# Performance work log

Hardware: AMD Instinct MI355X
Metric: run time of the kernel (lower is better)

## Reference

```python
import jax, jax.numpy as jnp
import numpy as np

N = 50000
E = 800000
D_IN = 128
D_H = 128
N_CLASSES = 40
N_HIDDEN = 2


def _gcn_norm(edge_index, num_nodes):
    # Add self loops, compute symmetric normalization D^-1/2 (A+I) D^-1/2
    loops = jnp.arange(num_nodes, dtype=edge_index.dtype)
    src = jnp.concatenate([edge_index[0], loops])
    dst = jnp.concatenate([edge_index[1], loops])
    deg = jax.ops.segment_sum(jnp.ones_like(src, dtype=jnp.float32), dst,
                              num_segments=num_nodes)
    dinv = jnp.where(deg > 0, jax.lax.rsqrt(jnp.maximum(deg, 1.0)), 0.0)
    norm = dinv[src] * dinv[dst]  # [E+N]
    return src, dst, norm


def _gcn_conv(x, src, dst, norm, W, b):
    h = x @ W                          # [N, d_out] transform first (PyG order)
    msg = h[src] * norm[:, None]       # gather + scale, [E+N, d_out]
    out = jax.ops.segment_sum(msg, dst, num_segments=x.shape[0])
    return out + b


def setup_inputs() -> dict:
    key = jax.random.key(0)
    ks = jax.random.split(key, 8)
    x = jax.random.normal(ks[0], (N, D_IN), dtype=jnp.float32)
    edge_index = jax.random.randint(ks[1], (2, E), 0, N, dtype=jnp.int64)
    s = 1.0 / np.sqrt(D_IN)
    W1 = jax.random.uniform(ks[2], (D_IN, D_H), minval=-s, maxval=s, dtype=jnp.float32)
    b1 = jnp.zeros((D_H,), dtype=jnp.float32)
    sh = 1.0 / np.sqrt(D_H)
    Wh = jax.random.uniform(ks[3], (N_HIDDEN, D_H, D_H), minval=-sh, maxval=sh, dtype=jnp.float32)
    bh = jnp.zeros((N_HIDDEN, D_H), dtype=jnp.float32)
    Wf = jax.random.uniform(ks[4], (D_H, N_CLASSES), minval=-sh, maxval=sh, dtype=jnp.float32)
    bf = jnp.zeros((N_CLASSES,), dtype=jnp.float32)
    return {"x": x, "edge_index": edge_index, "W1": W1, "b1": b1,
            "Wh": Wh, "bh": bh, "Wf": Wf, "bf": bf}


def reference(x, edge_index, W1, b1, Wh, bh, Wf, bf):
    src, dst, norm = _gcn_norm(edge_index, x.shape[0])
    h = jax.nn.relu(_gcn_conv(x, src, dst, norm, W1, b1))
    for i in range(Wh.shape[0]):  # small fixed layer count
        h = jax.nn.relu(_gcn_conv(h, src, dst, norm, Wh[i], bh[i]))
    # extra relu in original forward is a no-op after relu above
    return h @ Wf + bf
```

## Files before the change

### kernel.cpp

```cpp
#include <hip/hip_runtime.h>

#define D 128
#define NC 40

typedef __attribute__((ext_vector_type(8))) short short8v;
typedef __attribute__((ext_vector_type(4))) float f32x4;

__device__ __forceinline__ unsigned short f2bf(float f) {
    unsigned u = __float_as_uint(f);
    u += 0x7fff + ((u >> 16) & 1);
    return (unsigned short)(u >> 16);
}
__device__ __forceinline__ float bf2f(unsigned short h) {
    return __uint_as_float(((unsigned)h) << 16);
}

__device__ __forceinline__ int load_idx(const int* ei, long long pos, int is64) {
    return is64 ? ei[pos * 2] : ei[pos];
}

__device__ __forceinline__ int detect64(const int* __restrict__ ei) {
    int lane = threadIdx.x & 63;
    int hi = ei[lane * 2 + 1];
    return __any(hi != 0) ? 0 : 1;
}


__global__ void count_convert_kernel(const int* __restrict__ ei, int* __restrict__ deg,
                                     int E, int EB,
                                     const float* __restrict__ W1, const float* __restrict__ Wh,
                                     const float* __restrict__ Wf,
                                     unsigned short* __restrict__ Wc1, unsigned short* __restrict__ Wch0,
                                     unsigned short* __restrict__ Wch1, unsigned short* __restrict__ Wcf) {
    if (blockIdx.x < EB) {
        int is64 = detect64(ei);
        int e = blockIdx.x * 256 + threadIdx.x;
        if (e < E) {
            int d = load_idx(ei, (long long)E + e, is64);
            atomicAdd(&deg[d], 1);
        }
    } else {
        int idx = (blockIdx.x - EB) * 256 + threadIdx.x;
        if (idx < 49152) {
            int which = idx >> 14;
            int j = idx & 16383;
            int nn = j >> 7, k = j & 127;
            const float* W = (which == 0) ? W1 : (which == 1) ? Wh : Wh + 16384;
            unsigned short* o = (which == 0) ? Wc1 : (which == 1) ? Wch0 : Wch1;
            float v = W[k * 128 + nn];
            unsigned short h = f2bf(v);
            o[j] = h;
            o[16384 + j] = f2bf(v - bf2f(h));
        } else if (idx < 49152 + 6144) {
            int j = idx - 49152;
            int nn = j >> 7, k = j & 127;
            float v = (nn < NC) ? Wf[k * NC + nn] : 0.f;
            unsigned short h = f2bf(v);
            Wcf[j] = h;
            Wcf[6144 + j] = f2bf(v - bf2f(h));
        }
    }
}

__global__ void scan1_kernel(const int* __restrict__ deg, int* __restrict__ bsum, int m) {
    int i = blockIdx.x * 512 + threadIdx.x;
    int v = (i < m) ? deg[i] : 0;
    #pragma unroll
    for (int off = 32; off; off >>= 1) v += __shfl_down(v, off, 64);
    __shared__ int ws[8];
    if ((threadIdx.x & 63) == 0) ws[threadIdx.x >> 6] = v;
    __syncthreads();
    if (threadIdx.x == 0) {
        int s = 0;
        #pragma unroll
        for (int j = 0; j < 8; ++j) s += ws[j];
        bsum[blockIdx.x] = s;
    }
}

__global__ void scan3_kernel(const int* __restrict__ deg, const int* __restrict__ bsum,
                             int* __restrict__ rowptr, int* __restrict__ fill,
                             float* __restrict__ dinv, int n, int E, int nb) {
    int t = threadIdx.x;
    int lane = t & 63, w = t >> 6;
    int pv = (t < nb && t < (int)blockIdx.x) ? bsum[t] : 0;
    int rs = pv;
    #pragma unroll
    for (int off = 32; off; off >>= 1) rs += __shfl_down(rs, off, 64);
    __shared__ int red[8];
    if (lane == 0) red[w] = rs;
    __syncthreads();
    int base = 0;
    #pragma unroll
    for (int j = 0; j < 8; ++j) base += red[j];
    __syncthreads();

    int i = blockIdx.x * 512 + t;
    int v = (i < n) ? deg[i] : 0;
    int s = v;
    #pragma unroll
    for (int off = 1; off < 64; off <<= 1) {
        int x = __shfl_up(s, off, 64);
        if (lane >= off) s += x;
    }
    __shared__ int wsum[8];
    if (lane == 63) wsum[w] = s;
    __syncthreads();
    int wbase = 0;
    #pragma unroll
    for (int j = 0; j < 8; ++j) if (j < w) wbase += wsum[j];
    int excl = base + wbase + s - v;
    if (i < n) {
        rowptr[i] = excl;
        fill[i]   = excl;
        dinv[i]   = rsqrtf((float)(v + 1));
    }
    if (i == 0) rowptr[n] = E;
}

__global__ void scatter_kernel(const int* __restrict__ ei, int* __restrict__ fill,
                               const float* __restrict__ dinv, int2* __restrict__ col2, int E) {
    int is64 = detect64(ei);
    int e = blockIdx.x * 256 + threadIdx.x;
    if (e >= E) return;
    int s = load_idx(ei, (long long)e, is64);
    int d = load_idx(ei, (long long)E + e, is64);
    int pos = atomicAdd(&fill[d], 1);
    col2[pos] = make_int2(s, __float_as_int(dinv[s]));
}

__launch_bounds__(256)
__global__ void fused_layer_kernel(const float4* __restrict__ h4,
                                   const unsigned short* __restrict__ Wcvt,
                                   const float* __restrict__ bias,
                                   const float* __restrict__ dinv,
                                   const int* __restrict__ rowptr, const int2* __restrict__ col2,
                                   float* __restrict__ out, int n) {
    __shared__ unsigned short Ah[16 * 128];
    __shared__ unsigned short Al[16 * 128];
    int t = threadIdx.x;
    int g = t >> 4, l16 = t & 15;
    int node = blockIdx.x * 16 + g;
    int nd = (node < n) ? node : (n - 1);
    float dn = dinv[nd];
    size_t rowbase = (size_t)nd * 32;

    float4 a0 = h4[rowbase + l16];
    float4 a1 = h4[rowbase + l16 + 16];
    float4 acc0, acc1;
    acc0.x = a0.x * dn; acc0.y = a0.y * dn; acc0.z = a0.z * dn; acc0.w = a0.w * dn;
    acc1.x = a1.x * dn; acc1.y = a1.y * dn; acc1.z = a1.z * dn; acc1.w = a1.w * dn;

    int e = rowptr[nd], e1 = rowptr[nd + 1];
    for (; e + 4 <= e1; e += 4) {
        int2 c[4];
        #pragma unroll
        for (int j = 0; j < 4; ++j) c[j] = col2[e + j];
        float4 v0[4], v1[4];
        #pragma unroll
        for (int j = 0; j < 4; ++j) {
            size_t b = (size_t)c[j].x * 32;
            v0[j] = h4[b + l16];
            v1[j] = h4[b + l16 + 16];
        }
        #pragma unroll
        for (int j = 0; j < 4; ++j) {
            float ds = __int_as_float(c[j].y);
            acc0.x += v0[j].x * ds; acc0.y += v0[j].y * ds;
            acc0.z += v0[j].z * ds; acc0.w += v0[j].w * ds;
            acc1.x += v1[j].x * ds; acc1.y += v1[j].y * ds;
            acc1.z += v1[j].z * ds; acc1.w += v1[j].w * ds;
        }
    }
    for (; e < e1; ++e) {
        int2 c = col2[e];
        float ds = __int_as_float(c.y);
        size_t b = (size_t)c.x * 32;
        float4 v0 = h4[b + l16], v1 = h4[b + l16 + 16];
        acc0.x += v0.x * ds; acc0.y += v0.y * ds; acc0.z += v0.z * ds; acc0.w += v0.w * ds;
        acc1.x += v1.x * ds; acc1.y += v1.y * ds; acc1.z += v1.z * ds; acc1.w += v1.w * ds;
    }
    acc0.x *= dn; acc0.y *= dn; acc0.z *= dn; acc0.w *= dn;
    acc1.x *= dn; acc1.y *= dn; acc1.z *= dn; acc1.w *= dn;

    {
        int kc0 = l16 >> 1, sub = (l16 & 1) * 8;
        int off0 = (g << 8) + (((kc0) << 4) ^ ((g & 7) << 4)) + sub;
        int off1 = (g << 8) + (((kc0 + 8) << 4) ^ ((g & 7) << 4)) + sub;
        ushort4 h0, l0, h1, l1;
        h0.x = f2bf(acc0.x); l0.x = f2bf(acc0.x - bf2f(h0.x));
        h0.y = f2bf(acc0.y); l0.y = f2bf(acc0.y - bf2f(h0.y));
        h0.z = f2bf(acc0.z); l0.z = f2bf(acc0.z - bf2f(h0.z));
        h0.w = f2bf(acc0.w); l0.w = f2bf(acc0.w - bf2f(h0.w));
        h1.x = f2bf(acc1.x); l1.x = f2bf(acc1.x - bf2f(h1.x));
        h1.y = f2bf(acc1.y); l1.y = f2bf(acc1.y - bf2f(h1.y));
        h1.z = f2bf(acc1.z); l1.z = f2bf(acc1.z - bf2f(h1.z));
        h1.w = f2bf(acc1.w); l1.w = f2bf(acc1.w - bf2f(h1.w));
        *(ushort4*)((char*)Ah + off0) = h0;
        *(ushort4*)((char*)Al + off0) = l0;
        *(ushort4*)((char*)Ah + off1) = h1;
        *(ushort4*)((char*)Al + off1) = l1;
    }
    __syncthreads();

    int l = t & 63, wv = t >> 6;
    int lr = l & 15, lh = l >> 4;
    const unsigned short* Whi = Wcvt;
    const unsigned short* Wlo = Wcvt + 128 * 128;
    f32x4 o0 = (f32x4){0.f, 0.f, 0.f, 0.f};
    f32x4 o1 = (f32x4){0.f, 0.f, 0.f, 0.f};
    int n0 = wv * 32;
    #pragma unroll
    for (int ks = 0; ks < 4; ++ks) {
        int aoff = (lr << 8) + (((ks << 6) + (lh << 4)) ^ ((lr & 7) << 4));
        short8v ah = *(short8v*)((char*)Ah + aoff);
        short8v al = *(short8v*)((char*)Al + aoff);
        int c0 = (n0 + lr) * 128 + ks * 32 + lh * 8;
        int c1 = (n0 + 16 + lr) * 128 + ks * 32 + lh * 8;
        short8v bh0 = *(const short8v*)&Whi[c0];
        short8v bl0 = *(const short8v*)&Wlo[c0];
        short8v bh1 = *(const short8v*)&Whi[c1];
        short8v bl1 = *(const short8v*)&Wlo[c1];
        o0 = __builtin_amdgcn_mfma_f32_16x16x32_bf16(ah, bh0, o0, 0, 0, 0);
        o0 = __builtin_amdgcn_mfma_f32_16x16x32_bf16(ah, bl0, o0, 0, 0, 0);
        o0 = __builtin_amdgcn_mfma_f32_16x16x32_bf16(al, bh0, o0, 0, 0, 0);
        o1 = __builtin_amdgcn_mfma_f32_16x16x32_bf16(ah, bh1, o1, 0, 0, 0);
        o1 = __builtin_amdgcn_mfma_f32_16x16x32_bf16(ah, bl1, o1, 0, 0, 0);
        o1 = __builtin_amdgcn_mfma_f32_16x16x32_bf16(al, bh1, o1, 0, 0, 0);
    }
    float b0 = bias[n0 + lr], b1v = bias[n0 + 16 + lr];
    #pragma unroll
    for (int r = 0; r < 4; ++r) {
        int row = blockIdx.x * 16 + lh * 4 + r;
        if (row < n) {
            out[(size_t)row * 128 + n0 + lr]      = fmaxf(o0[r] + b0, 0.f);
            out[(size_t)row * 128 + n0 + 16 + lr] = fmaxf(o1[r] + b1v, 0.f);
        }
    }
}

__launch_bounds__(256)
__global__ void final_mfma_kernel(const float* __restrict__ A, const unsigned short* __restrict__ Wcvt,
                                  const float* __restrict__ bf, float* __restrict__ C, int M) {
    __shared__ unsigned short Ah[64 * 128];
    __shared__ unsigned short Al[64 * 128];
    int t = threadIdx.x;
    int l = t & 63, w = t >> 6;
    int lr = l & 15, lh = l >> 4;

    const unsigned short* Whi = Wcvt;
    const unsigned short* Wlo = Wcvt + 48 * 128;
    short8v bhi[3][4], blo[3][4];
    #pragma unroll
    for (int nt = 0; nt < 3; ++nt) {
        int n = nt * 16 + lr;
        #pragma unroll
        for (int ks = 0; ks < 4; ++ks) {
            bhi[nt][ks] = *(const short8v*)&Whi[n * 128 + ks * 32 + lh * 8];
            blo[nt][ks] = *(const short8v*)&Wlo[n * 128 + ks * 32 + lh * 8];
        }
    }

    int row0 = blockIdx.x * 64;
    #pragma unroll
    for (int c = 0; c < 4; ++c) {
        int chunk = c * 256 + t;
        int r  = chunk >> 4;
        int kc = chunk & 15;
        int gr = row0 + r; if (gr >= M) gr = M - 1;
        float4 a0 = *(const float4*)&A[(size_t)gr * 128 + kc * 8];
        float4 a1 = *(const float4*)&A[(size_t)gr * 128 + kc * 8 + 4];
        float av[8] = {a0.x, a0.y, a0.z, a0.w, a1.x, a1.y, a1.z, a1.w};
        short8v hv, lv;
        #pragma unroll
        for (int j = 0; j < 8; ++j) {
            unsigned short hi = f2bf(av[j]);
            hv[j] = (short)hi;
            lv[j] = (short)f2bf(av[j] - bf2f(hi));
        }
        int off = (r << 8) + ((kc << 4) ^ ((r & 7) << 4));
        *(short8v*)((char*)Ah + off) = hv;
        *(short8v*)((char*)Al + off) = lv;
    }
    __syncthreads();

    f32x4 acc[3];
    #pragma unroll
    for (int nt = 0; nt < 3; ++nt) acc[nt] = (f32x4){0.f, 0.f, 0.f, 0.f};
    int row = w * 16 + lr;
    #pragma unroll
    for (int ks = 0; ks < 4; ++ks) {
        int off = (row << 8) + (((ks << 6) + (lh << 4)) ^ ((row & 7) << 4));
        short8v ah = *(short8v*)((char*)Ah + off);
        short8v al = *(short8v*)((char*)Al + off);
        #pragma unroll
        for (int nt = 0; nt < 3; ++nt) {
            acc[nt] = __builtin_amdgcn_mfma_f32_16x16x32_bf16(ah, bhi[nt][ks], acc[nt], 0, 0, 0);
            acc[nt] = __builtin_amdgcn_mfma_f32_16x16x32_bf16(ah, blo[nt][ks], acc[nt], 0, 0, 0);
            acc[nt] = __builtin_amdgcn_mfma_f32_16x16x32_bf16(al, bhi[nt][ks], acc[nt], 0, 0, 0);
        }
    }
    #pragma unroll
    for (int nt = 0; nt < 3; ++nt) {
        int col = nt * 16 + lr;
        #pragma unroll
        for (int r = 0; r < 4; ++r) {
            int ro = row0 + w * 16 + lh * 4 + r;
            if (col < NC && ro < M) C[(size_t)ro * NC + col] = acc[nt][r] + bf[col];
        }
    }
}

extern "C" void kernel_launch(void* const* d_in, const int* in_sizes, int n_in,
                              void* d_out, int out_size, void* d_ws, size_t ws_size,
                              hipStream_t stream) {
    const float* x  = (const float*)d_in[0];
    const int*   ei = (const int*)d_in[1];
    const float* W1 = (const float*)d_in[2];
    const float* b1 = (const float*)d_in[3];
    const float* Wh = (const float*)d_in[4];
    const float* bh = (const float*)d_in[5];
    const float* Wf = (const float*)d_in[6];
    const float* bf = (const float*)d_in[7];
    float* out = (float*)d_out;

    int n = in_sizes[0] / D;
    int E = in_sizes[1] / 2;

    char* ws = (char*)d_ws;
    size_t off = 0;
    auto alloc = [&](size_t bytes) {
        void* p = ws + off;
        off = (off + bytes + 255) & ~(size_t)255;
        return p;
    };
    float* B0     = (float*)alloc((size_t)n * D * 4);
    float* B1     = (float*)alloc((size_t)n * D * 4);
    int*   deg    = (int*)alloc((size_t)n * 4);
    int*   rowptr = (int*)alloc((size_t)(n + 1) * 4);
    int*   fill   = (int*)alloc((size_t)n * 4);
    int2*  col2   = (int2*)alloc((size_t)E * 8);
    float* dinv   = (float*)alloc((size_t)n * 4);
    int*   bsum   = (int*)alloc(1024 * 4);
    unsigned short* Wc1  = (unsigned short*)alloc(2 * 128 * 128 * 2);
    unsigned short* Wch0 = (unsigned short*)alloc(2 * 128 * 128 * 2);
    unsigned short* Wch1 = (unsigned short*)alloc(2 * 128 * 128 * 2);
    unsigned short* Wcf  = (unsigned short*)alloc(2 * 48 * 128 * 2);

    int EB = (E + 255) / 256;
    int CB = (49152 + 6144 + 255) / 256;
    int nb = (n + 511) / 512;

    hipMemsetAsync(deg, 0, (size_t)n * 4, stream);
    count_convert_kernel<<<EB + CB, 256, 0, stream>>>(ei, deg, E, EB, W1, Wh, Wf, Wc1, Wch0, Wch1, Wcf);
    scan1_kernel<<<nb, 512, 0, stream>>>(deg, bsum, n);
    scan3_kernel<<<nb, 512, 0, stream>>>(deg, bsum, rowptr, fill, dinv, n, E, nb);
    scatter_kernel<<<EB, 256, 0, stream>>>(ei, fill, dinv, col2, E);

    int fgrid = (n + 15) / 16;

    fused_layer_kernel<<<fgrid, 256, 0, stream>>>((const float4*)x, Wc1, b1, dinv, rowptr, col2, B0, n);
    fused_layer_kernel<<<fgrid, 256, 0, stream>>>((const float4*)B0, Wch0, bh, dinv, rowptr, col2, B1, n);
    fused_layer_kernel<<<fgrid, 256, 0, stream>>>((const float4*)B1, Wch1, bh + D, dinv, rowptr, col2, B0, n);
    final_mfma_kernel<<<(n + 63) / 64, 256, 0, stream>>>(B0, Wcf, bf, out, n);
}
```

Baseline: 332.4 us.

## Use 32 lanes per node in fused GCN layer with 512-thread blocks

The fused aggregation+GEMM kernel now gives each node 32 threads, each loading one float4 per neighbor, instead of 16 threads loading two. Blocks grow to 512 threads, and each of the 8 waves computes one 16-column MFMA tile instead of two. An 8-way unrolled edge loop is added so more independent gathers are in flight. The goal is more memory-level parallelism and shorter per-thread dependency chains in the gather, which is latency-bound, at the cost of more threads per block and a heavier block-level barrier.

Measured after the change: 350.5 us. 5.4% more time.

```diff
diff --git a/kernel.cpp b/kernel.cpp
--- a/kernel.cpp
+++ b/kernel.cpp
@@ -129,7 +129,7 @@
     col2[pos] = make_int2(s, __float_as_int(dinv[s]));
 }
 
-__launch_bounds__(256)
+__launch_bounds__(512)
 __global__ void fused_layer_kernel(const float4* __restrict__ h4,
                                    const unsigned short* __restrict__ Wcvt,
                                    const float* __restrict__ bias,
@@ -139,103 +139,87 @@
     __shared__ unsigned short Ah[16 * 128];
     __shared__ unsigned short Al[16 * 128];
     int t = threadIdx.x;
-    int g = t >> 4, l16 = t & 15;
+    int g = t >> 5, l = t & 31;
     int node = blockIdx.x * 16 + g;
     int nd = (node < n) ? node : (n - 1);
     float dn = dinv[nd];
     size_t rowbase = (size_t)nd * 32;
 
-    float4 a0 = h4[rowbase + l16];
-    float4 a1 = h4[rowbase + l16 + 16];
-    float4 acc0, acc1;
-    acc0.x = a0.x * dn; acc0.y = a0.y * dn; acc0.z = a0.z * dn; acc0.w = a0.w * dn;
-    acc1.x = a1.x * dn; acc1.y = a1.y * dn; acc1.z = a1.z * dn; acc1.w = a1.w * dn;
-
+    float4 hv = h4[rowbase + l];
+    float4 acc;
+    acc.x = hv.x * dn; acc.y = hv.y * dn; acc.z = hv.z * dn; acc.w = hv.w * dn;
     int e = rowptr[nd], e1 = rowptr[nd + 1];
+    for (; e + 8 <= e1; e += 8) {
+        int2 c[8];
+        #pragma unroll
+        for (int j = 0; j < 8; ++j) c[j] = col2[e + j];
+        float4 v[8];
+        #pragma unroll
+        for (int j = 0; j < 8; ++j) v[j] = h4[(size_t)c[j].x * 32 + l];
+        #pragma unroll
+        for (int j = 0; j < 8; ++j) {
+            float ds = __int_as_float(c[j].y);
+            acc.x += v[j].x * ds; acc.y += v[j].y * ds;
+            acc.z += v[j].z * ds; acc.w += v[j].w * ds;
+        }
+    }
     for (; e + 4 <= e1; e += 4) {
         int2 c[4];
         #pragma unroll
         for (int j = 0; j < 4; ++j) c[j] = col2[e + j];
-        float4 v0[4], v1[4];
-        #pragma unroll
-        for (int j = 0; j < 4; ++j) {
-            size_t b = (size_t)c[j].x * 32;
-            v0[j] = h4[b + l16];
-            v1[j] = h4[b + l16 + 16];
-        }
+        float4 v[4];
+        #pragma unroll
+        for (int j = 0; j < 4; ++j) v[j] = h4[(size_t)c[j].x * 32 + l];
         #pragma unroll
         for (int j = 0; j < 4; ++j) {
             float ds = __int_as_float(c[j].y);
-            acc0.x += v0[j].x * ds; acc0.y += v0[j].y * ds;
-            acc0.z += v0[j].z * ds; acc0.w += v0[j].w * ds;
-            acc1.x += v1[j].x * ds; acc1.y += v1[j].y * ds;
-            acc1.z += v1[j].z * ds; acc1.w += v1[j].w * ds;
+            acc.x += v[j].x * ds; acc.y += v[j].y * ds;
+            acc.z += v[j].z * ds; acc.w += v[j].w * ds;
         }
     }
     for (; e < e1; ++e) {
         int2 c = col2[e];
         float ds = __int_as_float(c.y);
-        size_t b = (size_t)c.x * 32;
-        float4 v0 = h4[b + l16], v1 = h4[b + l16 + 16];
-        acc0.x += v0.x * ds; acc0.y += v0.y * ds; acc0.z += v0.z * ds; acc0.w += v0.w * ds;
-        acc1.x += v1.x * ds; acc1.y += v1.y * ds; acc1.z += v1.z * ds; acc1.w += v1.w * ds;
-    }
-    acc0.x *= dn; acc0.y *= dn; acc0.z *= dn; acc0.w *= dn;
-    acc1.x *= dn; acc1.y *= dn; acc1.z *= dn; acc1.w *= dn;
+        float4 v = h4[(size_t)c.x * 32 + l];
+        acc.x += v.x * ds; acc.y += v.y * ds; acc.z += v.z * ds; acc.w += v.w * ds;
+    }
+    acc.x *= dn; acc.y *= dn; acc.z *= dn; acc.w *= dn;
 
     {
-        int kc0 = l16 >> 1, sub = (l16 & 1) * 8;
-        int off0 = (g << 8) + (((kc0) << 4) ^ ((g & 7) << 4)) + sub;
-        int off1 = (g << 8) + (((kc0 + 8) << 4) ^ ((g & 7) << 4)) + sub;
-        ushort4 h0, l0, h1, l1;
-        h0.x = f2bf(acc0.x); l0.x = f2bf(acc0.x - bf2f(h0.x));
-        h0.y = f2bf(acc0.y); l0.y = f2bf(acc0.y - bf2f(h0.y));
-        h0.z = f2bf(acc0.z); l0.z = f2bf(acc0.z - bf2f(h0.z));
-        h0.w = f2bf(acc0.w); l0.w = f2bf(acc0.w - bf2f(h0.w));
-        h1.x = f2bf(acc1.x); l1.x = f2bf(acc1.x - bf2f(h1.x));
-        h1.y = f2bf(acc1.y); l1.y = f2bf(acc1.y - bf2f(h1.y));
-        h1.z = f2bf(acc1.z); l1.z = f2bf(acc1.z - bf2f(h1.z));
-        h1.w = f2bf(acc1.w); l1.w = f2bf(acc1.w - bf2f(h1.w));
-        *(ushort4*)((char*)Ah + off0) = h0;
-        *(ushort4*)((char*)Al + off0) = l0;
-        *(ushort4*)((char*)Ah + off1) = h1;
-        *(ushort4*)((char*)Al + off1) = l1;
-    }
-    __syncthreads();
-
-    int l = t & 63, wv = t >> 6;
-    int lr = l & 15, lh = l >> 4;
+        ushort4 hi, lo;
+        hi.x = f2bf(acc.x); lo.x = f2bf(acc.x - bf2f(hi.x));
+        hi.y = f2bf(acc.y); lo.y = f2bf(acc.y - bf2f(hi.y));
+        hi.z = f2bf(acc.z); lo.z = f2bf(acc.z - bf2f(hi.z));
+        hi.w = f2bf(acc.w); lo.w = f2bf(acc.w - bf2f(hi.w));
+        int off = (g << 8) + ((l << 3) ^ ((g & 7) << 4));
+        *(ushort4*)((char*)Ah + off) = hi;
+        *(ushort4*)((char*)Al + off) = lo;
+    }
+    __syncthreads();
+
+    int l64 = t & 63, wv = t >> 6;
+    int lr = l64 & 15, lh = l64 >> 4;
+    int n0 = wv * 16;
     const unsigned short* Whi = Wcvt;
     const unsigned short* Wlo = Wcvt + 128 * 128;
-    f32x4 o0 = (f32x4){0.f, 0.f, 0.f, 0.f};
-    f32x4 o1 = (f32x4){0.f, 0.f, 0.f, 0.f};
-    int n0 = wv * 32;
+    f32x4 o = (f32x4){0.f, 0.f, 0.f, 0.f};
     #pragma unroll
     for (int ks = 0; ks < 4; ++ks) {
         int aoff = (lr << 8) + (((ks << 6) + (lh << 4)) ^ ((lr & 7) << 4));
         short8v ah = *(short8v*)((char*)Ah + aoff);
         short8v al = *(short8v*)((char*)Al + aoff);
         int c0 = (n0 + lr) * 128 + ks * 32 + lh * 8;
-        int c1 = (n0 + 16 + lr) * 128 + ks * 32 + lh * 8;
-        short8v bh0 = *(const short8v*)&Whi[c0];
-        short8v bl0 = *(const short8v*)&Wlo[c0];
-        short8v bh1 = *(const short8v*)&Whi[c1];
-        short8v bl1 = *(const short8v*)&Wlo[c1];
-        o0 = __builtin_amdgcn_mfma_f32_16x16x32_bf16(ah, bh0, o0, 0, 0, 0);
-        o0 = __builtin_amdgcn_mfma_f32_16x16x32_bf16(ah, bl0, o0, 0, 0, 0);
-        o0 = __builtin_amdgcn_mfma_f32_16x16x32_bf16(al, bh0, o0, 0, 0, 0);
-        o1 = __builtin_amdgcn_mfma_f32_16x16x32_bf16(ah, bh1, o1, 0, 0, 0);
-        o1 = __builtin_amdgcn_mfma_f32_16x16x32_bf16(ah, bl1, o1, 0, 0, 0);
-        o1 = __builtin_amdgcn_mfma_f32_16x16x32_bf16(al, bh1, o1, 0, 0, 0);
-    }
-    float b0 = bias[n0 + lr], b1v = bias[n0 + 16 + lr];
+        short8v bh = *(const short8v*)&Whi[c0];
+        short8v bl = *(const short8v*)&Wlo[c0];
+        o = __builtin_amdgcn_mfma_f32_16x16x32_bf16(ah, bh, o, 0, 0, 0);
+        o = __builtin_amdgcn_mfma_f32_16x16x32_bf16(ah, bl, o, 0, 0, 0);
+        o = __builtin_amdgcn_mfma_f32_16x16x32_bf16(al, bh, o, 0, 0, 0);
+    }
+    float bv = bias[n0 + lr];
     #pragma unroll
     for (int r = 0; r < 4; ++r) {
         int row = blockIdx.x * 16 + lh * 4 + r;
-        if (row < n) {
-            out[(size_t)row * 128 + n0 + lr]      = fmaxf(o0[r] + b0, 0.f);
-            out[(size_t)row * 128 + n0 + 16 + lr] = fmaxf(o1[r] + b1v, 0.f);
-        }
+        if (row < n) out[(size_t)row * 128 + n0 + lr] = fmaxf(o[r] + bv, 0.f);
     }
 }
 
@@ -359,8 +343,8 @@
 
     int fgrid = (n + 15) / 16;
 
-    fused_layer_kernel<<<fgrid, 256, 0, stream>>>((const float4*)x, Wc1, b1, dinv, rowptr, col2, B0, n);
-    fused_layer_kernel<<<fgrid, 256, 0, stream>>>((const float4*)B0, Wch0, bh, dinv, rowptr, col2, B1, n);
-    fused_layer_kernel<<<fgrid, 256, 0, stream>>>((const float4*)B1, Wch1, bh + D, dinv, rowptr, col2, B0, n);
+    fused_layer_kernel<<<fgrid, 512, 0, stream>>>((const float4*)x, Wc1, b1, dinv, rowptr, col2, B0, n);
+    fused_layer_kernel<<<fgrid, 512, 0, stream>>>((const float4*)B0, Wch0, bh, dinv, rowptr, col2, B1, n);
+    fused_layer_kernel<<<fgrid, 512, 0, stream>>>((const float4*)B1, Wch1, bh + D, dinv, rowptr, col2, B0, n);
     final_mfma_kernel<<<(n + 63) / 64, 256, 0, stream>>>(B0, Wcf, bf, out, n);
 }
```
